# Kernel tuning notes

Measured on AMD Instinct MI355X. Metric: run time of the kernel, lower is better.

Reference implementation:

```python
import jax, jax.numpy as jnp
import numpy as np

N = 100000      # num nodes
E = 600000      # num edges
DIN = 64        # input_dim
DH = 128        # hidden_dim
G = 512         # num graphs
EPS = 1e-5      # BatchNorm eps


def setup_inputs() -> dict:
    key = jax.random.key(0)
    ks = jax.random.split(key, 12)
    x = jax.random.normal(ks[0], (N, DIN), jnp.float32)
    edge_index = jax.random.randint(ks[1], (2, E), 0, N)
    batch = jnp.sort(jax.random.randint(ks[2], (N,), 0, G))

    def w(k, shape):
        return (jax.random.normal(k, shape, jnp.float32) / np.float32(np.sqrt(shape[0])))

    inp = {"x": x, "edge_index": edge_index, "batch": batch}
    inp.update(
        W1=w(ks[3], (DIN, DH)), b1=jnp.zeros((DH,), jnp.float32),
        bn1_g=jnp.ones((DH,), jnp.float32), bn1_b=jnp.zeros((DH,), jnp.float32),
        bn1_m=jax.random.normal(ks[4], (DH,), jnp.float32) * 0.1,
        bn1_v=jnp.ones((DH,), jnp.float32),
        W2=w(ks[5], (DH, DH)), b2=jnp.zeros((DH,), jnp.float32),
        bn2_g=jnp.ones((DH,), jnp.float32), bn2_b=jnp.zeros((DH,), jnp.float32),
        bn2_m=jax.random.normal(ks[6], (DH,), jnp.float32) * 0.1,
        bn2_v=jnp.ones((DH,), jnp.float32),
        W3=w(ks[7], (DH, DH)), b3=jnp.zeros((DH,), jnp.float32),
        bn3_g=jnp.ones((DH,), jnp.float32), bn3_b=jnp.zeros((DH,), jnp.float32),
        bn3_m=jax.random.normal(ks[8], (DH,), jnp.float32) * 0.1,
        bn3_v=jnp.ones((DH,), jnp.float32),
        fc1_w=w(ks[9], (DH, DH // 2)), fc1_b=jnp.zeros((DH // 2,), jnp.float32),
        fc2_w=w(ks[10], (DH // 2, 1)), fc2_b=jnp.zeros((1,), jnp.float32),
    )
    return inp


def reference(x, edge_index, batch,
              W1, b1, bn1_g, bn1_b, bn1_m, bn1_v,
              W2, b2, bn2_g, bn2_b, bn2_m, bn2_v,
              W3, b3, bn3_g, bn3_b, bn3_m, bn3_v,
              fc1_w, fc1_b, fc2_w, fc2_b):
    # --- GCN normalization with self-loops (PyG GCNConv, sym norm) ---
    loop = jnp.arange(N, dtype=edge_index.dtype)
    src = jnp.concatenate([edge_index[0], loop])  # [E+N]
    dst = jnp.concatenate([edge_index[1], loop])  # [E+N]
    deg = jax.ops.segment_sum(jnp.ones_like(dst, jnp.float32), dst, num_segments=N)
    dis = jnp.where(deg > 0, jax.lax.rsqrt(jnp.maximum(deg, 1.0)), 0.0)
    norm = (dis[src] * dis[dst])[:, None]  # [E+N, 1]

    def conv(h, W, b):
        h = h @ W
        agg = jax.ops.segment_sum(h[src] * norm, dst, num_segments=N)
        return agg + b

    def bn(h, g, bta, m, v):
        return (h - m) * jax.lax.rsqrt(v + EPS) * g + bta  # eval-mode BatchNorm1d

    # block 1 (dropout is identity in eval)
    h = jax.nn.relu(bn(conv(x, W1, b1), bn1_g, bn1_b, bn1_m, bn1_v))
    # middle residual block (num_layers=3 -> one block)
    h = jax.nn.relu(bn(conv(h, W2, b2), bn2_g, bn2_b, bn2_m, bn2_v)) + h
    # output conv block
    h = jax.nn.relu(bn(conv(h, W3, b3), bn3_g, bn3_b, bn3_m, bn3_v))

    # global mean pool over graphs
    sums = jax.ops.segment_sum(h, batch, num_segments=G)          # [G, DH]
    cnt = jax.ops.segment_sum(jnp.ones((N, 1), h.dtype), batch, num_segments=G)
    pooled = sums / jnp.maximum(cnt, 1.0)

    h = jax.nn.relu(pooled @ fc1_w + fc1_b)
    return jax.nn.sigmoid(h @ fc2_w + fc2_b)  # [G, 1]
```

## Files before the change

### kernel.cpp

```cpp
#include <hip/hip_runtime.h>
#include <math.h>

#define N_NODES 100000
#define N_EDGES 600000
#define DIN     64
#define DH      128
#define NG      512
#define EPS_BN  1e-5f
#define SCAN_TPB 256
#define N_SCAN_BLK ((N_NODES + SCAN_TPB - 1) / SCAN_TPB)

typedef unsigned short u16;
typedef short s16x8 __attribute__((ext_vector_type(8)));
typedef float f32x4 __attribute__((ext_vector_type(4)));

__device__ __forceinline__ u16 f2bf(float x) {
    unsigned u = __builtin_bit_cast(unsigned, x);
    u += 0x7fffu + ((u >> 16) & 1u);
    return (u16)(u >> 16);
}
__device__ __forceinline__ float bf2f(u16 h) {
    unsigned u = ((unsigned)h) << 16;
    return __builtin_bit_cast(float, u);
}

__global__ __launch_bounds__(256) void deg_kernel(const int* __restrict__ dst,
                                                  float* __restrict__ deg, int E) {
    int e = blockIdx.x * blockDim.x + threadIdx.x;
    if (e < E) atomicAdd(&deg[dst[e]], 1.0f);
}

__global__ __launch_bounds__(256) void dis_kernel(const float* __restrict__ deg,
                                                  float* __restrict__ dis,
                                                  int* __restrict__ deg_i, int n) {
    int i = blockIdx.x * blockDim.x + threadIdx.x;
    if (i < n) {
        float d = deg[i];
        dis[i] = rsqrtf(d + 1.0f);
        deg_i[i] = (int)d;
    }
}

__global__ __launch_bounds__(SCAN_TPB) void scan1_kernel(const int* __restrict__ deg_i,
                                                         int* __restrict__ row_ptr,
                                                         int* __restrict__ blk, int n) {
    __shared__ int sm[SCAN_TPB];
    const int t = threadIdx.x;
    const int i = blockIdx.x * SCAN_TPB + t;
    const int v = (i < n) ? deg_i[i] : 0;
    sm[t] = v;
    __syncthreads();
#pragma unroll
    for (int off = 1; off < SCAN_TPB; off <<= 1) {
        int u = (t >= off) ? sm[t - off] : 0;
        __syncthreads();
        sm[t] += u;
        __syncthreads();
    }
    if (i < n) row_ptr[i] = sm[t] - v;
    if (t == SCAN_TPB - 1) blk[blockIdx.x] = sm[t];
}

__global__ __launch_bounds__(512) void scan2_kernel(int* __restrict__ blk,
                                                    int* __restrict__ row_ptr,
                                                    int nblk, int n) {
    __shared__ int sm[512];
    const int t = threadIdx.x;
    const int v = (t < nblk) ? blk[t] : 0;
    sm[t] = v;
    __syncthreads();
#pragma unroll
    for (int off = 1; off < 512; off <<= 1) {
        int u = (t >= off) ? sm[t - off] : 0;
        __syncthreads();
        sm[t] += u;
        __syncthreads();
    }
    if (t < nblk) blk[t] = sm[t] - v;
    if (t == nblk - 1) row_ptr[n] = sm[t];
}

__global__ __launch_bounds__(SCAN_TPB) void scan3_kernel(int* __restrict__ row_ptr,
                                                         const int* __restrict__ blk, int n) {
    const int i = blockIdx.x * SCAN_TPB + threadIdx.x;
    if (i < n) row_ptr[i] += blk[blockIdx.x];
}

__global__ __launch_bounds__(256) void build_csr_kernel(const int* __restrict__ src,
                                                        const int* __restrict__ dst,
                                                        const float* __restrict__ dis,
                                                        const int* __restrict__ row_ptr,
                                                        int* __restrict__ cursor,
                                                        int* __restrict__ col,
                                                        float* __restrict__ val, int E) {
    int e = blockIdx.x * blockDim.x + threadIdx.x;
    if (e >= E) return;
    const int s = src[e];
    const int d = dst[e];
    const int p = atomicAdd(&cursor[d], 1);
    const int idx = row_ptr[d] + p;
    col[idx] = s;
    val[idx] = dis[s] * dis[d];
}

__global__ __launch_bounds__(256) void xcvt_kernel(const float* __restrict__ x,
                                                   u16* __restrict__ xb, long n) {
    long i = ((long)blockIdx.x * blockDim.x + threadIdx.x) * 8;
    if (i >= n) return;
    const float4 a = *(const float4*)(x + i);
    const float4 b = *(const float4*)(x + i + 4);
    s16x8 o;
    o[0] = (short)f2bf(a.x); o[1] = (short)f2bf(a.y);
    o[2] = (short)f2bf(a.z); o[3] = (short)f2bf(a.w);
    o[4] = (short)f2bf(b.x); o[5] = (short)f2bf(b.y);
    o[6] = (short)f2bf(b.z); o[7] = (short)f2bf(b.w);
    *(s16x8*)(xb + i) = o;
}

__global__ __launch_bounds__(256) void wt_kernel(const float* __restrict__ W,
                                                 u16* __restrict__ Wt, int K, int N) {
    int idx = blockIdx.x * blockDim.x + threadIdx.x;
    if (idx >= K * N) return;
    int k = idx / N, n = idx % N;
    Wt[(long)n * K + k] = f2bf(W[idx]);
}

__global__ __launch_bounds__(256) void bn_prep_kernel(
    const float* b1, const float* g1, const float* bb1, const float* m1, const float* v1,
    const float* b2, const float* g2, const float* bb2, const float* m2, const float* v2,
    const float* b3, const float* g3, const float* bb3, const float* m3, const float* v3,
    float* __restrict__ sc, float* __restrict__ sh) {
    int i = blockIdx.x * blockDim.x + threadIdx.x;
    if (i >= 3 * DH) return;
    int l = i >> 7, c = i & (DH - 1);
    const float* bc = l == 0 ? b1 : (l == 1 ? b2 : b3);
    const float* g  = l == 0 ? g1 : (l == 1 ? g2 : g3);
    const float* bb = l == 0 ? bb1 : (l == 1 ? bb2 : bb3);
    const float* m  = l == 0 ? m1 : (l == 1 ? m2 : m3);
    const float* v  = l == 0 ? v1 : (l == 1 ? v2 : v3);
    float s = g[c] * rsqrtf(v[c] + EPS_BN);
    sc[i] = s;
    sh[i] = (bc[c] - m[c]) * s + bb[c];
}

template <int K>
__global__ __launch_bounds__(256) void gemm_mfma(const u16* __restrict__ A,
                                                 const u16* __restrict__ Wt,
                                                 u16* __restrict__ C,
                                                 int M) {
    const int wave = threadIdx.x >> 6;
    const int lane = threadIdx.x & 63;
    const int r16 = lane & 15;
    const int kc  = lane >> 4;
    const long row0 = (long)blockIdx.x * 64 + wave * 16;

    f32x4 acc[8];
#pragma unroll
    for (int t = 0; t < 8; ++t)
#pragma unroll
        for (int q = 0; q < 4; ++q) acc[t][q] = 0.0f;

    long arow = row0 + r16;
    if (arow >= M) arow = M - 1;
    const u16* ap = A + arow * K + kc * 8;

#pragma unroll
    for (int ks = 0; ks < K; ks += 32) {
        const s16x8 a = *(const s16x8*)(ap + ks);
#pragma unroll
        for (int t = 0; t < 8; ++t) {
            const s16x8 b = *(const s16x8*)(Wt + (long)(t * 16 + r16) * K + ks + kc * 8);
            acc[t] = __builtin_amdgcn_mfma_f32_16x16x32_bf16(a, b, acc[t], 0, 0, 0);
        }
    }

#pragma unroll
    for (int r = 0; r < 4; ++r) {
        const long row = row0 + kc * 4 + r;
        if (row < M) {
            u16* cp = C + row * DH + r16;
#pragma unroll
            for (int t = 0; t < 8; ++t) cp[t * 16] = f2bf(acc[t][r]);
        }
    }
}

template <bool RES>
__global__ __launch_bounds__(256) void agg_epi_kernel(const u16* __restrict__ H,
                                                      const int* __restrict__ row_ptr,
                                                      const int* __restrict__ col,
                                                      const float* __restrict__ val,
                                                      const float* __restrict__ dis,
                                                      const float* __restrict__ scl,
                                                      const float* __restrict__ shf,
                                                      u16* __restrict__ out, int n) {
    const long t = (long)blockIdx.x * blockDim.x + threadIdx.x;
    const int lane = (int)(t & 15);
    const long i = t >> 4;
    if (i >= n) return;
    const int c = lane * 8;

    float d2 = dis[i];
    d2 *= d2;
    float acc[8];
    const s16x8 hv = *(const s16x8*)(H + i * DH + c);
#pragma unroll
    for (int q = 0; q < 8; ++q) acc[q] = bf2f((u16)hv[q]) * d2;

    const int beg = row_ptr[i];
    const int end = row_ptr[i + 1];
    for (int e = beg; e < end; ++e) {
        const int s = col[e];
        const float nm = val[e];
        const s16x8 v = *(const s16x8*)(H + (long)s * DH + c);
#pragma unroll
        for (int q = 0; q < 8; ++q) acc[q] = fmaf(bf2f((u16)v[q]), nm, acc[q]);
    }

    const float4 s0 = *(const float4*)(scl + c);
    const float4 s1 = *(const float4*)(scl + c + 4);
    const float4 f0 = *(const float4*)(shf + c);
    const float4 f1 = *(const float4*)(shf + c + 4);
    const float sv[8] = {s0.x, s0.y, s0.z, s0.w, s1.x, s1.y, s1.z, s1.w};
    const float fv[8] = {f0.x, f0.y, f0.z, f0.w, f1.x, f1.y, f1.z, f1.w};

    float r[8];
#pragma unroll
    for (int q = 0; q < 8; ++q) r[q] = fmaxf(fmaf(acc[q], sv[q], fv[q]), 0.0f);
    if (RES) {
        const s16x8 rv = *(const s16x8*)(out + i * DH + c);
#pragma unroll
        for (int q = 0; q < 8; ++q) r[q] += bf2f((u16)rv[q]);
    }
    s16x8 ov;
#pragma unroll
    for (int q = 0; q < 8; ++q) ov[q] = (short)f2bf(r[q]);
    *(s16x8*)(out + i * DH + c) = ov;
}

__global__ __launch_bounds__(256) void graph_bounds_kernel(const int* __restrict__ batch,
                                                           int* __restrict__ gp) {
    int g = blockIdx.x * blockDim.x + threadIdx.x;
    if (g > NG) return;
    int lo = 0, hi = N_NODES;
    while (lo < hi) {
        int mid = (lo + hi) >> 1;
        if (batch[mid] < g) lo = mid + 1; else hi = mid;
    }
    gp[g] = lo;
}

__global__ __launch_bounds__(256) void pool_kernel(const u16* __restrict__ h,
                                                   const int* __restrict__ gp,
                                                   float* __restrict__ pooled) {
    const int g = blockIdx.x;
    const int t = threadIdx.x;
    const int grp = t >> 4;
    const int cl = t & 15;
    const int c = cl * 8;
    const int beg = gp[g];
    const int end = gp[g + 1];

    float acc[8] = {0, 0, 0, 0, 0, 0, 0, 0};
    for (int i = beg + grp; i < end; i += 16) {
        const s16x8 v = *(const s16x8*)(h + (long)i * DH + c);
#pragma unroll
        for (int q = 0; q < 8; ++q) acc[q] += bf2f((u16)v[q]);
    }

    __shared__ float sm[16][DH];
#pragma unroll
    for (int q = 0; q < 8; ++q) sm[grp][c + q] = acc[q];
    __syncthreads();

    if (t < DH) {
        float s = 0.0f;
#pragma unroll
        for (int r = 0; r < 16; ++r) s += sm[r][t];
        pooled[(long)g * DH + t] = s / fmaxf((float)(end - beg), 1.0f);
    }
}

__global__ __launch_bounds__(64) void head_kernel(const float* __restrict__ pooled,
                                                  const float* __restrict__ fc1w,
                                                  const float* __restrict__ fc1b,
                                                  const float* __restrict__ fc2w,
                                                  const float* __restrict__ fc2b,
                                                  float* __restrict__ out) {
    const int g = blockIdx.x;
    const int j = threadIdx.x;
    __shared__ float p[DH];
    p[j]      = pooled[(long)g * DH + j];
    p[j + 64] = pooled[(long)g * DH + 64 + j];
    __syncthreads();

    float acc = 0.0f;
#pragma unroll 4
    for (int k = 0; k < DH; ++k) acc = fmaf(p[k], fc1w[(long)k * 64 + j], acc);
    const float h1 = fmaxf(acc + fc1b[j], 0.0f);
    float v = h1 * fc2w[j];
#pragma unroll
    for (int off = 32; off > 0; off >>= 1) v += __shfl_down(v, off);
    if (j == 0) out[g] = 1.0f / (1.0f + expf(-(v + fc2b[0])));
}

extern "C" void kernel_launch(void* const* d_in, const int* in_sizes, int n_in,
                              void* d_out, int out_size, void* d_ws, size_t ws_size,
                              hipStream_t stream) {
    const float* x     = (const float*)d_in[0];
    const int*   ei    = (const int*)d_in[1];
    const int*   batch = (const int*)d_in[2];
    const float* W1 = (const float*)d_in[3];
    const float* b1 = (const float*)d_in[4];
    const float* g1 = (const float*)d_in[5];
    const float* t1 = (const float*)d_in[6];
    const float* m1 = (const float*)d_in[7];
    const float* v1 = (const float*)d_in[8];
    const float* W2 = (const float*)d_in[9];
    const float* b2 = (const float*)d_in[10];
    const float* g2 = (const float*)d_in[11];
    const float* t2 = (const float*)d_in[12];
    const float* m2 = (const float*)d_in[13];
    const float* v2 = (const float*)d_in[14];
    const float* W3 = (const float*)d_in[15];
    const float* b3 = (const float*)d_in[16];
    const float* g3 = (const float*)d_in[17];
    const float* t3 = (const float*)d_in[18];
    const float* m3 = (const float*)d_in[19];
    const float* v3 = (const float*)d_in[20];
    const float* fc1w = (const float*)d_in[21];
    const float* fc1b = (const float*)d_in[22];
    const float* fc2w = (const float*)d_in[23];
    const float* fc2b = (const float*)d_in[24];

    const int* src = ei;
    const int* dst = ei + N_EDGES;

    char* ws = (char*)d_ws;
    size_t off = 0;
    auto alloc = [&](size_t bytes) -> char* {
        char* p = ws + off;
        off = (off + bytes + 511) & ~(size_t)511;
        return p;
    };
    float* deg     = (float*)alloc((size_t)N_NODES * 4);
    float* dis     = (float*)alloc((size_t)N_NODES * 4);
    int*   deg_i   = (int*)  alloc((size_t)N_NODES * 4);
    int*   row_ptr = (int*)  alloc(((size_t)N_NODES + 1) * 4);
    int*   cursor  = (int*)  alloc((size_t)N_NODES * 4);
    int*   blk     = (int*)  alloc((size_t)N_SCAN_BLK * 4);
    int*   col     = (int*)  alloc((size_t)N_EDGES * 4);
    float* val     = (float*)alloc((size_t)N_EDGES * 4);
    int*   gp      = (int*)  alloc((size_t)(NG + 1) * 4);
    float* pooled  = (float*)alloc((size_t)NG * DH * 4);
    float* bnsc    = (float*)alloc((size_t)3 * DH * 4);
    float* bnsh    = (float*)alloc((size_t)3 * DH * 4);
    u16*   xb      = (u16*)  alloc((size_t)N_NODES * DIN * 2);
    u16*   Wt1     = (u16*)  alloc((size_t)DH * DIN * 2);
    u16*   Wt2     = (u16*)  alloc((size_t)DH * DH * 2);
    u16*   Wt3     = (u16*)  alloc((size_t)DH * DH * 2);
    u16*   bufB    = (u16*)  alloc((size_t)N_NODES * DH * 2);
    u16*   bufA    = (u16*)  alloc((size_t)N_NODES * DH * 2);

    const int TPB = 256;
    const int gEdge  = (N_EDGES + TPB - 1) / TPB;
    const int gNode  = (N_NODES + TPB - 1) / TPB;
    const int gGemm  = (N_NODES + 63) / 64;
    const int gAgg   = (int)(((long)N_NODES * 16 + TPB - 1) / TPB);

    hipMemsetAsync(deg, 0, (size_t)N_NODES * 4, stream);
    hipMemsetAsync(cursor, 0, (size_t)N_NODES * 4, stream);
    deg_kernel<<<gEdge, TPB, 0, stream>>>(dst, deg, N_EDGES);
    dis_kernel<<<gNode, TPB, 0, stream>>>(deg, dis, deg_i, N_NODES);
    scan1_kernel<<<N_SCAN_BLK, SCAN_TPB, 0, stream>>>(deg_i, row_ptr, blk, N_NODES);
    scan2_kernel<<<1, 512, 0, stream>>>(blk, row_ptr, N_SCAN_BLK, N_NODES);
    scan3_kernel<<<N_SCAN_BLK, SCAN_TPB, 0, stream>>>(row_ptr, blk, N_NODES);
    build_csr_kernel<<<gEdge, TPB, 0, stream>>>(src, dst, dis, row_ptr, cursor, col, val,
                                                N_EDGES);
    graph_bounds_kernel<<<3, 256, 0, stream>>>(batch, gp);

    xcvt_kernel<<<(int)(((long)N_NODES * DIN / 8 + TPB - 1) / TPB), TPB, 0, stream>>>(
        x, xb, (long)N_NODES * DIN);
    wt_kernel<<<(DIN * DH + TPB - 1) / TPB, TPB, 0, stream>>>(W1, Wt1, DIN, DH);
    wt_kernel<<<(DH * DH + TPB - 1) / TPB, TPB, 0, stream>>>(W2, Wt2, DH, DH);
    wt_kernel<<<(DH * DH + TPB - 1) / TPB, TPB, 0, stream>>>(W3, Wt3, DH, DH);
    bn_prep_kernel<<<2, TPB, 0, stream>>>(b1, g1, t1, m1, v1, b2, g2, t2, m2, v2,
                                          b3, g3, t3, m3, v3, bnsc, bnsh);

    gemm_mfma<DIN><<<gGemm, TPB, 0, stream>>>(xb, Wt1, bufB, N_NODES);
    agg_epi_kernel<false><<<gAgg, TPB, 0, stream>>>(bufB, row_ptr, col, val, dis,
                                                    bnsc, bnsh, bufA, N_NODES);
    gemm_mfma<DH><<<gGemm, TPB, 0, stream>>>(bufA, Wt2, bufB, N_NODES);
    agg_epi_kernel<true><<<gAgg, TPB, 0, stream>>>(bufB, row_ptr, col, val, dis,
                                                   bnsc + DH, bnsh + DH, bufA, N_NODES);
    gemm_mfma<DH><<<gGemm, TPB, 0, stream>>>(bufA, Wt3, bufB, N_NODES);
    agg_epi_kernel<false><<<gAgg, TPB, 0, stream>>>(bufB, row_ptr, col, val, dis,
                                                    bnsc + 2 * DH, bnsh + 2 * DH, bufA,
                                                    N_NODES);

    pool_kernel<<<NG, TPB, 0, stream>>>(bufA, gp, pooled);
    head_kernel<<<NG, 64, 0, stream>>>(pooled, fc1w, fc1b, fc2w, fc2b, (float*)d_out);
}
```

Measured before the change: 319.6 us.

## Split edge loop across two half-warps, pack CSR col/val, fuse prep kernels

The aggregation kernel now gives each node 32 lanes instead of 16. Two 16-lane halves each process alternate edges, and their partial sums are combined with a cross-lane shuffle. This adds memory-level parallelism on the gather. Column index and normalization weight are packed into a single 64-bit entry, so each edge needs one load instead of two. The x conversion, weight transposes, BN prep and graph-bounds kernels are merged into one launch, and the two memsets become one, to cut launch overhead. The cost is more threads per node and idle lanes in the epilogue.

New measurement: 310.3 us. -2.9%, faster.

```diff
diff --git a/kernel.cpp b/kernel.cpp
--- a/kernel.cpp
+++ b/kernel.cpp
@@ -11,6 +11,7 @@
 #define N_SCAN_BLK ((N_NODES + SCAN_TPB - 1) / SCAN_TPB)
 
 typedef unsigned short u16;
+typedef unsigned long long u64;
 typedef short s16x8 __attribute__((ext_vector_type(8)));
 typedef float f32x4 __attribute__((ext_vector_type(4)));
 
@@ -91,56 +92,88 @@
                                                         const float* __restrict__ dis,
                                                         const int* __restrict__ row_ptr,
                                                         int* __restrict__ cursor,
-                                                        int* __restrict__ col,
-                                                        float* __restrict__ val, int E) {
+                                                        u64* __restrict__ colval, int E) {
     int e = blockIdx.x * blockDim.x + threadIdx.x;
     if (e >= E) return;
     const int s = src[e];
     const int d = dst[e];
     const int p = atomicAdd(&cursor[d], 1);
-    const int idx = row_ptr[d] + p;
-    col[idx] = s;
-    val[idx] = dis[s] * dis[d];
-}
-
-__global__ __launch_bounds__(256) void xcvt_kernel(const float* __restrict__ x,
-                                                   u16* __restrict__ xb, long n) {
-    long i = ((long)blockIdx.x * blockDim.x + threadIdx.x) * 8;
-    if (i >= n) return;
-    const float4 a = *(const float4*)(x + i);
-    const float4 b = *(const float4*)(x + i + 4);
-    s16x8 o;
-    o[0] = (short)f2bf(a.x); o[1] = (short)f2bf(a.y);
-    o[2] = (short)f2bf(a.z); o[3] = (short)f2bf(a.w);
-    o[4] = (short)f2bf(b.x); o[5] = (short)f2bf(b.y);
-    o[6] = (short)f2bf(b.z); o[7] = (short)f2bf(b.w);
-    *(s16x8*)(xb + i) = o;
-}
-
-__global__ __launch_bounds__(256) void wt_kernel(const float* __restrict__ W,
-                                                 u16* __restrict__ Wt, int K, int N) {
-    int idx = blockIdx.x * blockDim.x + threadIdx.x;
-    if (idx >= K * N) return;
-    int k = idx / N, n = idx % N;
+    const unsigned fb = __builtin_bit_cast(unsigned, dis[s] * dis[d]);
+    colval[row_ptr[d] + p] = ((u64)fb << 32) | (unsigned)s;
+}
+
+#define PREP_XCVT_BLKS 3125
+#define PREP_WT1_BLKS  32
+#define PREP_WT2_BLKS  64
+#define PREP_WT3_BLKS  64
+#define PREP_BN_BLKS   2
+#define PREP_GB_BLKS   3
+#define PREP_B0 PREP_XCVT_BLKS
+#define PREP_B1 (PREP_B0 + PREP_WT1_BLKS)
+#define PREP_B2 (PREP_B1 + PREP_WT2_BLKS)
+#define PREP_B3 (PREP_B2 + PREP_WT3_BLKS)
+#define PREP_B4 (PREP_B3 + PREP_BN_BLKS)
+#define PREP_TOTAL (PREP_B4 + PREP_GB_BLKS)
+
+__device__ __forceinline__ void wt_body(const float* __restrict__ W, u16* __restrict__ Wt,
+                                        int K, int idx) {
+    if (idx >= K * DH) return;
+    int k = idx / DH, n = idx % DH;
     Wt[(long)n * K + k] = f2bf(W[idx]);
 }
 
-__global__ __launch_bounds__(256) void bn_prep_kernel(
+__global__ __launch_bounds__(256) void prep_kernel(
+    const float* __restrict__ x, u16* __restrict__ xb,
+    const float* __restrict__ W1, u16* __restrict__ Wt1,
+    const float* __restrict__ W2, u16* __restrict__ Wt2,
+    const float* __restrict__ W3, u16* __restrict__ Wt3,
     const float* b1, const float* g1, const float* bb1, const float* m1, const float* v1,
     const float* b2, const float* g2, const float* bb2, const float* m2, const float* v2,
     const float* b3, const float* g3, const float* bb3, const float* m3, const float* v3,
-    float* __restrict__ sc, float* __restrict__ sh) {
-    int i = blockIdx.x * blockDim.x + threadIdx.x;
-    if (i >= 3 * DH) return;
-    int l = i >> 7, c = i & (DH - 1);
-    const float* bc = l == 0 ? b1 : (l == 1 ? b2 : b3);
-    const float* g  = l == 0 ? g1 : (l == 1 ? g2 : g3);
-    const float* bb = l == 0 ? bb1 : (l == 1 ? bb2 : bb3);
-    const float* m  = l == 0 ? m1 : (l == 1 ? m2 : m3);
-    const float* v  = l == 0 ? v1 : (l == 1 ? v2 : v3);
-    float s = g[c] * rsqrtf(v[c] + EPS_BN);
-    sc[i] = s;
-    sh[i] = (bc[c] - m[c]) * s + bb[c];
+    float* __restrict__ sc, float* __restrict__ sh,
+    const int* __restrict__ batch, int* __restrict__ gp) {
+    const int b = blockIdx.x;
+    const int tid = threadIdx.x;
+    if (b < PREP_B0) {
+        const long i = ((long)b * 256 + tid) * 8;
+        const float4 a = *(const float4*)(x + i);
+        const float4 c = *(const float4*)(x + i + 4);
+        s16x8 o;
+        o[0] = (short)f2bf(a.x); o[1] = (short)f2bf(a.y);
+        o[2] = (short)f2bf(a.z); o[3] = (short)f2bf(a.w);
+        o[4] = (short)f2bf(c.x); o[5] = (short)f2bf(c.y);
+        o[6] = (short)f2bf(c.z); o[7] = (short)f2bf(c.w);
+        *(s16x8*)(xb + i) = o;
+    } else if (b < PREP_B1) {
+        wt_body(W1, Wt1, DIN, (b - PREP_B0) * 256 + tid);
+    } else if (b < PREP_B2) {
+        wt_body(W2, Wt2, DH, (b - PREP_B1) * 256 + tid);
+    } else if (b < PREP_B3) {
+        wt_body(W3, Wt3, DH, (b - PREP_B2) * 256 + tid);
+    } else if (b < PREP_B4) {
+        const int i = (b - PREP_B3) * 256 + tid;
+        if (i < 3 * DH) {
+            int l = i >> 7, c = i & (DH - 1);
+            const float* bc = l == 0 ? b1 : (l == 1 ? b2 : b3);
+            const float* g  = l == 0 ? g1 : (l == 1 ? g2 : g3);
+            const float* bb = l == 0 ? bb1 : (l == 1 ? bb2 : bb3);
+            const float* m  = l == 0 ? m1 : (l == 1 ? m2 : m3);
+            const float* v  = l == 0 ? v1 : (l == 1 ? v2 : v3);
+            float s = g[c] * rsqrtf(v[c] + EPS_BN);
+            sc[i] = s;
+            sh[i] = (bc[c] - m[c]) * s + bb[c];
+        }
+    } else {
+        const int g = (b - PREP_B4) * 256 + tid;
+        if (g <= NG) {
+            int lo = 0, hi = N_NODES;
+            while (lo < hi) {
+                int mid = (lo + hi) >> 1;
+                if (batch[mid] < g) lo = mid + 1; else hi = mid;
+            }
+            gp[g] = lo;
+        }
+    }
 }
 
 template <int K>
@@ -188,66 +221,63 @@
 template <bool RES>
 __global__ __launch_bounds__(256) void agg_epi_kernel(const u16* __restrict__ H,
                                                       const int* __restrict__ row_ptr,
-                                                      const int* __restrict__ col,
-                                                      const float* __restrict__ val,
+                                                      const u64* __restrict__ colval,
                                                       const float* __restrict__ dis,
                                                       const float* __restrict__ scl,
                                                       const float* __restrict__ shf,
                                                       u16* __restrict__ out, int n) {
     const long t = (long)blockIdx.x * blockDim.x + threadIdx.x;
-    const int lane = (int)(t & 15);
-    const long i = t >> 4;
+    const int lane = (int)(t & 31);
+    const long i = t >> 5;
     if (i >= n) return;
-    const int c = lane * 8;
-
-    float d2 = dis[i];
-    d2 *= d2;
-    float acc[8];
-    const s16x8 hv = *(const s16x8*)(H + i * DH + c);
-#pragma unroll
-    for (int q = 0; q < 8; ++q) acc[q] = bf2f((u16)hv[q]) * d2;
+    const int cl = lane & 15;
+    const int eh = lane >> 4;
+    const int c = cl * 8;
+
+    float acc[8] = {0, 0, 0, 0, 0, 0, 0, 0};
+    if (eh == 0) {
+        float d2 = dis[i];
+        d2 *= d2;
+        const s16x8 hv = *(const s16x8*)(H + i * DH + c);
+#pragma unroll
+        for (int q = 0; q < 8; ++q) acc[q] = bf2f((u16)hv[q]) * d2;
+    }
 
     const int beg = row_ptr[i];
     const int end = row_ptr[i + 1];
-    for (int e = beg; e < end; ++e) {
-        const int s = col[e];
-        const float nm = val[e];
+    for (int e = beg + eh; e < end; e += 2) {
+        const u64 cv = colval[e];
+        const int s = (int)(unsigned)cv;
+        const float nm = __builtin_bit_cast(float, (unsigned)(cv >> 32));
         const s16x8 v = *(const s16x8*)(H + (long)s * DH + c);
 #pragma unroll
         for (int q = 0; q < 8; ++q) acc[q] = fmaf(bf2f((u16)v[q]), nm, acc[q]);
     }
 
-    const float4 s0 = *(const float4*)(scl + c);
-    const float4 s1 = *(const float4*)(scl + c + 4);
-    const float4 f0 = *(const float4*)(shf + c);
-    const float4 f1 = *(const float4*)(shf + c + 4);
-    const float sv[8] = {s0.x, s0.y, s0.z, s0.w, s1.x, s1.y, s1.z, s1.w};
-    const float fv[8] = {f0.x, f0.y, f0.z, f0.w, f1.x, f1.y, f1.z, f1.w};
-
-    float r[8];
-#pragma unroll
-    for (int q = 0; q < 8; ++q) r[q] = fmaxf(fmaf(acc[q], sv[q], fv[q]), 0.0f);
-    if (RES) {
-        const s16x8 rv = *(const s16x8*)(out + i * DH + c);
-#pragma unroll
-        for (int q = 0; q < 8; ++q) r[q] += bf2f((u16)rv[q]);
-    }
-    s16x8 ov;
-#pragma unroll
-    for (int q = 0; q < 8; ++q) ov[q] = (short)f2bf(r[q]);
-    *(s16x8*)(out + i * DH + c) = ov;
-}
-
-__global__ __launch_bounds__(256) void graph_bounds_kernel(const int* __restrict__ batch,
-                                                           int* __restrict__ gp) {
-    int g = blockIdx.x * blockDim.x + threadIdx.x;
-    if (g > NG) return;
-    int lo = 0, hi = N_NODES;
-    while (lo < hi) {
-        int mid = (lo + hi) >> 1;
-        if (batch[mid] < g) lo = mid + 1; else hi = mid;
-    }
-    gp[g] = lo;
+#pragma unroll
+    for (int q = 0; q < 8; ++q) acc[q] += __shfl_xor(acc[q], 16);
+
+    if (eh == 0) {
+        const float4 s0 = *(const float4*)(scl + c);
+        const float4 s1 = *(const float4*)(scl + c + 4);
+        const float4 f0 = *(const float4*)(shf + c);
+        const float4 f1 = *(const float4*)(shf + c + 4);
+        const float sv[8] = {s0.x, s0.y, s0.z, s0.w, s1.x, s1.y, s1.z, s1.w};
+        const float fv[8] = {f0.x, f0.y, f0.z, f0.w, f1.x, f1.y, f1.z, f1.w};
+
+        float r[8];
+#pragma unroll
+        for (int q = 0; q < 8; ++q) r[q] = fmaxf(fmaf(acc[q], sv[q], fv[q]), 0.0f);
+        if (RES) {
+            const s16x8 rv = *(const s16x8*)(out + i * DH + c);
+#pragma unroll
+            for (int q = 0; q < 8; ++q) r[q] += bf2f((u16)rv[q]);
+        }
+        s16x8 ov;
+#pragma unroll
+        for (int q = 0; q < 8; ++q) ov[q] = (short)f2bf(r[q]);
+        *(s16x8*)(out + i * DH + c) = ov;
+    }
 }
 
 __global__ __launch_bounds__(256) void pool_kernel(const u16* __restrict__ h,
@@ -343,14 +373,13 @@
         off = (off + bytes + 511) & ~(size_t)511;
         return p;
     };
-    float* deg     = (float*)alloc((size_t)N_NODES * 4);
+    float* deg     = (float*)alloc((size_t)2 * N_NODES * 4);
+    int*   cursor  = (int*)(deg + N_NODES);
     float* dis     = (float*)alloc((size_t)N_NODES * 4);
     int*   deg_i   = (int*)  alloc((size_t)N_NODES * 4);
     int*   row_ptr = (int*)  alloc(((size_t)N_NODES + 1) * 4);
-    int*   cursor  = (int*)  alloc((size_t)N_NODES * 4);
     int*   blk     = (int*)  alloc((size_t)N_SCAN_BLK * 4);
-    int*   col     = (int*)  alloc((size_t)N_EDGES * 4);
-    float* val     = (float*)alloc((size_t)N_EDGES * 4);
+    u64*   colval  = (u64*)  alloc((size_t)N_EDGES * 8);
     int*   gp      = (int*)  alloc((size_t)(NG + 1) * 4);
     float* pooled  = (float*)alloc((size_t)NG * DH * 4);
     float* bnsc    = (float*)alloc((size_t)3 * DH * 4);
@@ -366,35 +395,30 @@
     const int gEdge  = (N_EDGES + TPB - 1) / TPB;
     const int gNode  = (N_NODES + TPB - 1) / TPB;
     const int gGemm  = (N_NODES + 63) / 64;
-    const int gAgg   = (int)(((long)N_NODES * 16 + TPB - 1) / TPB);
-
-    hipMemsetAsync(deg, 0, (size_t)N_NODES * 4, stream);
-    hipMemsetAsync(cursor, 0, (size_t)N_NODES * 4, stream);
+    const int gAgg   = (int)(((long)N_NODES * 32 + TPB - 1) / TPB);
+
+    hipMemsetAsync(deg, 0, (size_t)2 * N_NODES * 4, stream);
     deg_kernel<<<gEdge, TPB, 0, stream>>>(dst, deg, N_EDGES);
     dis_kernel<<<gNode, TPB, 0, stream>>>(deg, dis, deg_i, N_NODES);
     scan1_kernel<<<N_SCAN_BLK, SCAN_TPB, 0, stream>>>(deg_i, row_ptr, blk, N_NODES);
     scan2_kernel<<<1, 512, 0, stream>>>(blk, row_ptr, N_SCAN_BLK, N_NODES);
     scan3_kernel<<<N_SCAN_BLK, SCAN_TPB, 0, stream>>>(row_ptr, blk, N_NODES);
-    build_csr_kernel<<<gEdge, TPB, 0, stream>>>(src, dst, dis, row_ptr, cursor, col, val,
+    build_csr_kernel<<<gEdge, TPB, 0, stream>>>(src, dst, dis, row_ptr, cursor, colval,
                                                 N_EDGES);
-    graph_bounds_kernel<<<3, 256, 0, stream>>>(batch, gp);
-
-    xcvt_kernel<<<(int)(((long)N_NODES * DIN / 8 + TPB - 1) / TPB), TPB, 0, stream>>>(
-        x, xb, (long)N_NODES * DIN);
-    wt_kernel<<<(DIN * DH + TPB - 1) / TPB, TPB, 0, stream>>>(W1, Wt1, DIN, DH);
-    wt_kernel<<<(DH * DH + TPB - 1) / TPB, TPB, 0, stream>>>(W2, Wt2, DH, DH);
-    wt_kernel<<<(DH * DH + TPB - 1) / TPB, TPB, 0, stream>>>(W3, Wt3, DH, DH);
-    bn_prep_kernel<<<2, TPB, 0, stream>>>(b1, g1, t1, m1, v1, b2, g2, t2, m2, v2,
-                                          b3, g3, t3, m3, v3, bnsc, bnsh);
+    prep_kernel<<<PREP_TOTAL, TPB, 0, stream>>>(x, xb, W1, Wt1, W2, Wt2, W3, Wt3,
+                                                b1, g1, t1, m1, v1,
+                                                b2, g2, t2, m2, v2,
+                                                b3, g3, t3, m3, v3,
+                                                bnsc, bnsh, batch, gp);
 
     gemm_mfma<DIN><<<gGemm, TPB, 0, stream>>>(xb, Wt1, bufB, N_NODES);
-    agg_epi_kernel<false><<<gAgg, TPB, 0, stream>>>(bufB, row_ptr, col, val, dis,
+    agg_epi_kernel<false><<<gAgg, TPB, 0, stream>>>(bufB, row_ptr, colval, dis,
                                                     bnsc, bnsh, bufA, N_NODES);
     gemm_mfma<DH><<<gGemm, TPB, 0, stream>>>(bufA, Wt2, bufB, N_NODES);
-    agg_epi_kernel<true><<<gAgg, TPB, 0, stream>>>(bufB, row_ptr, col, val, dis,
+    agg_epi_kernel<true><<<gAgg, TPB, 0, stream>>>(bufB, row_ptr, colval, dis,
                                                    bnsc + DH, bnsh + DH, bufA, N_NODES);
     gemm_mfma<DH><<<gGemm, TPB, 0, stream>>>(bufA, Wt3, bufB, N_NODES);
-    agg_epi_kernel<false><<<gAgg, TPB, 0, stream>>>(bufB, row_ptr, col, val, dis,
+    agg_epi_kernel<false><<<gAgg, TPB, 0, stream>>>(bufB, row_ptr, colval, dis,
                                                     bnsc + 2 * DH, bnsh + 2 * DH, bufA,
                                                     N_NODES);
 
```
